# Performance work log

Hardware: AMD Instinct MI355X
Metric: run time of the kernel (lower is better)

Reference implementation:

```python
import jax, jax.numpy as jnp
import numpy as np

NUM_EXPERTS = 8
TOP_K = 2
ROUTE_SCALE = 1.0
DIM = 1024
HID = 1024
B, S = 2, 4096


def setup_inputs() -> dict:
    key = jax.random.key(0)
    ks = jax.random.split(key, 9)
    sc = 0.05
    return {
        "x": jax.random.normal(ks[0], (B, S, DIM), dtype=jnp.float32),
        "gate_w": jax.random.normal(ks[1], (NUM_EXPERTS, DIM), dtype=jnp.float32) * sc,
        "w1": jax.random.normal(ks[2], (NUM_EXPERTS, HID, DIM), dtype=jnp.float32) * sc,
        "w2": jax.random.normal(ks[3], (NUM_EXPERTS, DIM, HID), dtype=jnp.float32) * sc,
        "w3": jax.random.normal(ks[4], (NUM_EXPERTS, HID, DIM), dtype=jnp.float32) * sc,
        "sw1": jax.random.normal(ks[5], (HID, DIM), dtype=jnp.float32) * sc,
        "sw2": jax.random.normal(ks[6], (DIM, HID), dtype=jnp.float32) * sc,
        "sw3": jax.random.normal(ks[7], (HID, DIM), dtype=jnp.float32) * sc,
        "expert_bias": jnp.zeros((NUM_EXPERTS,), dtype=jnp.float32),
    }


def reference(x, gate_w, w1, w2, w3, sw1, sw2, sw3, expert_bias):
    bs, slen, dim = x.shape
    xf = x.reshape(-1, dim)                      # [T, D]

    # ---- router (sigmoid scoring, top-k over scores + bias, gather true scores) ----
    scores = jax.nn.sigmoid((xf @ gate_w.T).astype(jnp.float32))   # [T, E]
    _, sel = jax.lax.top_k(scores + expert_bias[None, :], TOP_K)    # [T, K] int32
    top_scores = jnp.take_along_axis(scores, sel, axis=1) * ROUTE_SCALE  # [T, K]

    # ---- stable sort token-slots by chosen expert (dispatch permutation) ----
    flat_sel = sel.reshape(-1)                       # [T*K]
    order = jnp.argsort(flat_sel, stable=True)       # [T*K]
    scores_sorted = top_scores.reshape(-1)[order]    # [T*K]
    tok_idx = order // TOP_K                         # source token per slot
    expert_ids = flat_sel[order]                     # sorted expert id per slot

    routed = xf[tok_idx]                             # gather [T*K, D]
    # score_before_experts=True: scale inputs by routing score
    routed = (routed.astype(jnp.float32) * scores_sorted[:, None]).astype(x.dtype)

    # ---- grouped expert GLU MLP (loop over fixed expert count, masked) ----
    out_r = jnp.zeros_like(routed)
    for e in range(NUM_EXPERTS):
        m = (expert_ids == e)[:, None]
        h = jax.nn.silu(routed @ w1[e].T) * (routed @ w3[e].T)   # [T*K, H]
        out_r = out_r + jnp.where(m, h @ w2[e].T, jnp.zeros((), routed.dtype))

    # ---- shared expert on all tokens ----
    shared = (jax.nn.silu(xf @ sw1.T) * (xf @ sw3.T)) @ sw2.T    # [T, D]

    # NOTE: original code multiplies by routing scores again after experts
    # (in addition to score_before_experts) -- replicated faithfully.
    out_r = (out_r.astype(jnp.float32) * scores_sorted[:, None]).astype(x.dtype)

    out = shared.at[tok_idx].add(out_r)              # scatter-add combine
    return out.reshape(bs, slen, dim)
```

## Files before the change

kernel.cpp:

```cpp
#include <hip/hip_runtime.h>
#include <stdint.h>

typedef unsigned short u16;
typedef unsigned int u32;

#define T_TOK 8192
#define DIMSZ 1024
#define HIDSZ 1024
#define NE 8
#define NSLOT (T_TOK * 2)
#define NPAD (NSLOT + 1024)

typedef __attribute__((ext_vector_type(8))) __bf16 bf16x8;
typedef __attribute__((ext_vector_type(16))) float f32x16;

#define MFMA32(a, b, c) __builtin_amdgcn_mfma_f32_32x32x16_bf16(a, b, c, 0, 0, 0)

__device__ __forceinline__ size_t ablk(int pos, int c) {
  return ((((size_t)(pos >> 7) * 32 + (c >> 5)) * 4 + ((c >> 3) & 3)) * 128 +
          (pos & 127)) * 8 + (c & 7);
}

__device__ __forceinline__ u16 f2bf(float f) {
  u32 u = __builtin_bit_cast(u32, f);
  u += 0x7FFFu + ((u >> 16) & 1u);
  return (u16)(u >> 16);
}
__device__ __forceinline__ float bflo(u32 v) { return __builtin_bit_cast(float, v << 16); }
__device__ __forceinline__ float bfhi(u32 v) { return __builtin_bit_cast(float, v & 0xffff0000u); }
__device__ __forceinline__ u32 pack2(float a, float b) {
  return (u32)f2bf(a) | ((u32)f2bf(b) << 16);
}
__device__ __forceinline__ float silu_f(float v) { return v / (1.f + expf(-v)); }

__device__ __forceinline__ void gload16(const void* g, void* l) {
  __builtin_amdgcn_global_load_lds(
      (const __attribute__((address_space(1))) unsigned int*)g,
      (__attribute__((address_space(3))) unsigned int*)l, 16, 0, 0);
}

#define PIPE_SYNC(N) asm volatile("s_waitcnt vmcnt(" #N ")\n\ts_barrier" ::: "memory")

__global__ __launch_bounds__(256) void convert_blocked(
    const float* __restrict__ s0, const float* __restrict__ s1,
    const float* __restrict__ s2, const float* __restrict__ ss0,
    const float* __restrict__ ss1, const float* __restrict__ ss2,
    u16* __restrict__ d0, u16* __restrict__ d1, u16* __restrict__ d2,
    u16* __restrict__ ds0, u16* __restrict__ ds1, u16* __restrict__ ds2) {
  __shared__ u16 lt[2048];
  int t = blockIdx.x;
  const float* s;
  u16* d;
  if (t < NE * 16 * 32) {
    s = (blockIdx.y == 0) ? s0 : (blockIdx.y == 1) ? s1 : s2;
    d = (blockIdx.y == 0) ? d0 : (blockIdx.y == 1) ? d1 : d2;
  } else {
    t -= NE * 16 * 32;
    s = (blockIdx.y == 0) ? ss0 : (blockIdx.y == 1) ? ss1 : ss2;
    d = (blockIdx.y == 0) ? ds0 : (blockIdx.y == 1) ? ds1 : ds2;
  }
  int rt = t >> 5, kt = t & 31;
  const float* sp = s + (size_t)rt * 64 * 1024 + kt * 32;
  int nl = threadIdx.x >> 2, k0 = (threadIdx.x & 3) * 8;
  float4 a = *(const float4*)(sp + (size_t)nl * 1024 + k0);
  float4 b = *(const float4*)(sp + (size_t)nl * 1024 + k0 + 4);
  uint4 p;
  p.x = pack2(a.x, a.y); p.y = pack2(a.z, a.w);
  p.z = pack2(b.x, b.y); p.w = pack2(b.z, b.w);
  *(uint4*)&lt[(threadIdx.x & 3) * 512 + nl * 8] = p;
  __syncthreads();
  *(uint4*)(d + (size_t)t * 2048 + threadIdx.x * 8) = *(const uint4*)&lt[threadIdx.x * 8];
}

__global__ __launch_bounds__(256) void router_kernel(
    const float* __restrict__ x, const float* __restrict__ gw,
    const float* __restrict__ bias, int* __restrict__ sel,
    float* __restrict__ selscore, u16* __restrict__ xb) {
  int t = blockIdx.x * 4 + (threadIdx.x >> 6);
  int lane = threadIdx.x & 63;
  float a[NE];
#pragma unroll
  for (int e = 0; e < NE; e++) a[e] = 0.f;
#pragma unroll
  for (int j = 0; j < 4; j++) {
    int c = j * 256 + lane * 4;
    float4 xv = *(const float4*)&x[(size_t)t * DIMSZ + c];
    uint2 p;
    p.x = pack2(xv.x, xv.y);
    p.y = pack2(xv.z, xv.w);
    *(uint2*)&xb[ablk(t, c)] = p;
#pragma unroll
    for (int e = 0; e < NE; e++) {
      float4 gv = *(const float4*)&gw[e * DIMSZ + c];
      a[e] = fmaf(xv.x, gv.x, fmaf(xv.y, gv.y, fmaf(xv.z, gv.z, fmaf(xv.w, gv.w, a[e]))));
    }
  }
#pragma unroll
  for (int off = 1; off < 64; off <<= 1)
#pragma unroll
    for (int e = 0; e < NE; e++) a[e] += __shfl_xor(a[e], off);
  if (lane == 0) {
    float s[NE], b[NE];
#pragma unroll
    for (int e = 0; e < NE; e++) {
      s[e] = 1.f / (1.f + expf(-a[e]));
      b[e] = s[e] + bias[e];
    }
    int e1 = 0; float v1 = b[0];
#pragma unroll
    for (int e = 1; e < NE; e++) if (b[e] > v1) { v1 = b[e]; e1 = e; }
    int e2 = -1; float v2 = -1e30f;
#pragma unroll
    for (int e = 0; e < NE; e++) if (e != e1 && b[e] > v2) { v2 = b[e]; e2 = e; }
    sel[t * 2] = e1; sel[t * 2 + 1] = e2;
    selscore[t * 2] = s[e1];
    selscore[t * 2 + 1] = s[e2];
  }
}

__global__ __launch_bounds__(1024) void rank_kernel(
    const int* __restrict__ sel, const float* __restrict__ selscore,
    int* __restrict__ slot2pos, float* __restrict__ slot_score,
    int* __restrict__ counts, int* __restrict__ offsets) {
  __shared__ int hist[NE * 1024];
  __shared__ int tot[NE];
  __shared__ int offs[NE];
  int tid = threadIdx.x;
  int sl[16];
  int h[NE];
#pragma unroll
  for (int e = 0; e < NE; e++) h[e] = 0;
#pragma unroll
  for (int j = 0; j < 4; j++) {
    int4 v = ((const int4*)sel)[tid * 4 + j];
    sl[j * 4 + 0] = v.x; sl[j * 4 + 1] = v.y;
    sl[j * 4 + 2] = v.z; sl[j * 4 + 3] = v.w;
  }
#pragma unroll
  for (int i = 0; i < 16; i++)
#pragma unroll
    for (int e = 0; e < NE; e++) h[e] += (sl[i] == e) ? 1 : 0;
#pragma unroll
  for (int e = 0; e < NE; e++) hist[e * 1024 + tid] = h[e];
  __syncthreads();
  int wid = tid >> 6, lane = tid & 63;
  if (wid < NE) {
    int e = wid;
    int vals[16];
    int lsum = 0;
#pragma unroll
    for (int i = 0; i < 16; i++) {
      int v = hist[e * 1024 + lane * 16 + i];
      vals[i] = lsum;
      lsum += v;
    }
    int incl = lsum;
#pragma unroll
    for (int off = 1; off < 64; off <<= 1) {
      int v = __shfl_up(incl, off);
      if (lane >= off) incl += v;
    }
    int excl = incl - lsum;
#pragma unroll
    for (int i = 0; i < 16; i++) hist[e * 1024 + lane * 16 + i] = vals[i] + excl;
    if (lane == 63) tot[e] = incl;
  }
  __syncthreads();
  if (tid == 0) {
    int acc = 0;
    for (int e = 0; e < NE; e++) {
      offs[e] = acc;
      offsets[e] = acc;
      counts[e] = tot[e];
      acc += (tot[e] + 127) & ~127;
    }
  }
  __syncthreads();
  int base[NE];
#pragma unroll
  for (int e = 0; e < NE; e++) base[e] = offs[e] + hist[e * 1024 + tid];
#pragma unroll
  for (int i = 0; i < 16; i++) {
    int slot = tid * 16 + i;
    int e = sl[i];
    int pos = 0;
#pragma unroll
    for (int k = 0; k < NE; k++) pos += (e == k) ? base[k] : 0;
#pragma unroll
    for (int k = 0; k < NE; k++) base[k] += (e == k) ? 1 : 0;
    slot2pos[slot] = pos;
    slot_score[pos] = selscore[slot];
  }
}

__global__ __launch_bounds__(256) void gather_kernel(
    const u16* __restrict__ xb, const float* __restrict__ selscore,
    const int* __restrict__ slot2pos, u16* __restrict__ routed) {
  int s = blockIdx.x * 4 + (threadIdx.x >> 6);
  int lane = threadIdx.x & 63;
  int pos = slot2pos[s];
  float sc = selscore[s];
  int t = s >> 1;
#pragma unroll
  for (int j = 0; j < 4; j++) {
    int c = j * 256 + lane * 4;
    uint2 v = *(const uint2*)&xb[ablk(t, c)];
    uint2 p;
    p.x = pack2(bflo(v.x) * sc, bfhi(v.x) * sc);
    p.y = pack2(bflo(v.y) * sc, bfhi(v.y) * sc);
    *(uint2*)&routed[ablk(pos, c)] = p;
  }
}

#define BUFE 12288

#define PIPE_STAGE(B)                                  \
  do {                                                 \
    u16* Lb = &lds[(B) * BUFE];                        \
    gload16(pAa, Lb + tid * 8);                        \
    gload16(pAa + 2048, Lb + 2048 + tid * 8);          \
    gload16(pAb, Lb + 4096 + tid * 8);                 \
    gload16(pAb + 2048, Lb + 6144 + tid * 8);          \
    gload16(pBu0, Lb + 8192 + tid * 8);                \
    gload16(pBu1, Lb + 10240 + tid * 8);               \
    pAa += 4096; pAb += 4096; pBu0 += 2048; pBu1 += 2048; \
  } while (0)

#define PIPE_COMPUTE(B)                                                  \
  do {                                                                   \
    _Pragma("unroll")                                                    \
    for (int c = 0; c < 2; c++) {                                        \
      int kc = 2 * c + l5;                                               \
      const u16* La = &lds[(B) * BUFE] + wy * 4096 + kc * 1024;          \
      const u16* Lw = &lds[(B) * BUFE] + 8192 + wn * 2048 + kc * 512;    \
      bf16x8 b0 = *(const bf16x8*)&Lw[l31 * 8];                          \
      bf16x8 b1 = *(const bf16x8*)&Lw[256 + l31 * 8];                    \
      bf16x8 a0 = *(const bf16x8*)&La[l31 * 8];                          \
      acc[0][0] = MFMA32(a0, b0, acc[0][0]);                             \
      acc[0][1] = MFMA32(a0, b1, acc[0][1]);                             \
      bf16x8 a1 = *(const bf16x8*)&La[256 + l31 * 8];                    \
      acc[1][0] = MFMA32(a1, b0, acc[1][0]);                             \
      acc[1][1] = MFMA32(a1, b1, acc[1][1]);                             \
      bf16x8 a2 = *(const bf16x8*)&La[512 + l31 * 8];                    \
      acc[2][0] = MFMA32(a2, b0, acc[2][0]);                             \
      acc[2][1] = MFMA32(a2, b1, acc[2][1]);                             \
      bf16x8 a3 = *(const bf16x8*)&La[768 + l31 * 8];                    \
      acc[3][0] = MFMA32(a3, b0, acc[3][0]);                             \
      acc[3][1] = MFMA32(a3, b1, acc[3][1]);                             \
    }                                                                    \
  } while (0)

#define PIPE_PHASE(SB, CB)                  \
  PIPE_SYNC(6);                             \
  PIPE_STAGE(SB);                           \
  __builtin_amdgcn_s_setprio(1);            \
  PIPE_COMPUTE(CB);                         \
  __builtin_amdgcn_s_setprio(0);

#define PIPE_LOOP()                         \
  PIPE_STAGE(0);                            \
  PIPE_STAGE(1);                            \
  _Pragma("unroll 1")                       \
  for (int t = 0; t < 30; t += 3) {         \
    PIPE_PHASE(2, 0);                       \
    PIPE_PHASE(0, 1);                       \
    PIPE_PHASE(1, 2);                       \
  }                                         \
  PIPE_SYNC(6);                             \
  __builtin_amdgcn_s_setprio(1);            \
  PIPE_COMPUTE(0);                          \
  __builtin_amdgcn_s_setprio(0);            \
  PIPE_SYNC(0);                             \
  __builtin_amdgcn_s_setprio(1);            \
  PIPE_COMPUTE(1);                          \
  __builtin_amdgcn_s_setprio(0);

__global__ __launch_bounds__(256, 2) void dual_glu_gemm(
    const u16* __restrict__ A, const u16* __restrict__ W1,
    const u16* __restrict__ W3, u16* __restrict__ Hout,
    const u16* __restrict__ As, const u16* __restrict__ SW1,
    const u16* __restrict__ SW3, u16* __restrict__ Hs,
    const int* __restrict__ seg_off, const int* __restrict__ seg_cnt) {
  int flat = blockIdx.x + 16 * blockIdx.y + 512 * blockIdx.z;
  int xcd = flat & 7;
  int r = flat >> 3;
  int bx = r & 15;
  int s = r >> 4;
  int z, by;
  if (s < 4) { z = NE; by = xcd * 4 + s; }
  else       { z = xcd; by = s - 4; }

  const u16 *Ap, *w1p, *w3p;
  u16* Hp;
  int soff, scnt;
  if (z < NE) {
    soff = seg_off[z]; scnt = seg_cnt[z];
    Ap = A;
    w1p = W1 + (size_t)z * HIDSZ * DIMSZ;
    w3p = W3 + (size_t)z * HIDSZ * DIMSZ;
    Hp = Hout;
  } else {
    soff = 0; scnt = T_TOK;
    Ap = As; w1p = SW1; w3p = SW3;
    Hp = Hs;
  }
  int mbase = by * 256;
  if (mbase >= scnt) return;
  int hx = bx;

  __shared__ u16 lds[3 * BUFE];

  int tid = threadIdx.x;
  int lane = tid & 63;
  int wid = tid >> 6;
  int wy = wid >> 1, wn = wid & 1;
  int l5 = lane >> 5, l31 = lane & 31;

  const u16* pAa = Ap + (size_t)((soff + mbase) >> 7) * 32 * 4096 + tid * 8;
  const u16* pAb = pAa + 32 * 4096;
  const u16* pBu0 = w1p + (size_t)hx * 32 * 2048 + tid * 8;
  const u16* pBu1 = w3p + (size_t)hx * 32 * 2048 + tid * 8;

  f32x16 acc[4][2];
#pragma unroll
  for (int i = 0; i < 4; i++) { acc[i][0] = (f32x16)0.f; acc[i][1] = (f32x16)0.f; }

  PIPE_LOOP();

  __syncthreads();
  float* ex = (float*)lds;
  if (wn == 0) {
#pragma unroll
    for (int i = 0; i < 4; i++)
#pragma unroll
      for (int j = 0; j < 2; j++)
#pragma unroll
        for (int r2 = 0; r2 < 16; r2++) {
          int rowl = i * 32 + (r2 & 3) + 8 * (r2 >> 2) + 4 * l5;
          ex[(wy * 128 + rowl) * 64 + j * 32 + l31] = acc[i][j][r2];
        }
  }
  __syncthreads();
  if (wn == 1) {
#pragma unroll
    for (int i = 0; i < 4; i++)
#pragma unroll
      for (int j = 0; j < 2; j++)
#pragma unroll
        for (int r2 = 0; r2 < 16; r2++) {
          int rowl = i * 32 + (r2 & 3) + 8 * (r2 >> 2) + 4 * l5;
          int grow = mbase + wy * 128 + rowl;
          if (grow < scnt) {
            float h1 = ex[(wy * 128 + rowl) * 64 + j * 32 + l31];
            Hp[ablk(soff + grow, hx * 64 + j * 32 + l31)] =
                f2bf(silu_f(h1) * acc[i][j][r2]);
          }
        }
  }
}

__global__ __launch_bounds__(256, 2) void gemm2_kernel(
    const u16* __restrict__ A, const u16* __restrict__ W, u16* __restrict__ OutB,
    const u16* __restrict__ As, const u16* __restrict__ SW, float* __restrict__ OutF,
    const float* __restrict__ scale, const int* __restrict__ seg_off,
    const int* __restrict__ seg_cnt) {
  int flat = blockIdx.x + 8 * blockIdx.y + 256 * blockIdx.z;
  int xcd = flat & 7;
  int r = flat >> 3;
  int bx = r & 7;
  int s = r >> 3;
  int z, by;
  if (s < 4) { z = NE; by = xcd * 4 + s; }
  else       { z = xcd; by = s - 4; }

  const u16 *Ap, *wp;
  int soff, scnt;
  if (z < NE) {
    soff = seg_off[z]; scnt = seg_cnt[z];
    Ap = A; wp = W + (size_t)z * DIMSZ * HIDSZ;
  } else {
    soff = 0; scnt = T_TOK;
    Ap = As; wp = SW;
  }
  int mbase = by * 256;
  if (mbase >= scnt) return;
  int nbase = bx * 128;

  __shared__ u16 lds[3 * BUFE];

  int tid = threadIdx.x;
  int lane = tid & 63;
  int wid = tid >> 6;
  int wy = wid >> 1, wn = wid & 1;
  int l5 = lane >> 5, l31 = lane & 31;

  const u16* pAa = Ap + (size_t)((soff + mbase) >> 7) * 32 * 4096 + tid * 8;
  const u16* pAb = pAa + 32 * 4096;
  const u16* pBu0 = wp + (size_t)(nbase >> 6) * 32 * 2048 + tid * 8;
  const u16* pBu1 = pBu0 + 32 * 2048;

  f32x16 acc[4][2];
#pragma unroll
  for (int i = 0; i < 4; i++) { acc[i][0] = (f32x16)0.f; acc[i][1] = (f32x16)0.f; }

  PIPE_LOOP();

#pragma unroll
  for (int i = 0; i < 4; i++)
#pragma unroll
    for (int j = 0; j < 2; j++) {
      int colg = nbase + wn * 64 + j * 32 + l31;
#pragma unroll
      for (int r2 = 0; r2 < 16; r2++) {
        int rowl = (r2 & 3) + 8 * (r2 >> 2) + 4 * l5;
        int grow = mbase + wy * 128 + i * 32 + rowl;
        if (grow < scnt) {
          size_t idx = (size_t)(soff + grow) * DIMSZ + colg;
          if (z < NE) {
            OutB[idx] = f2bf(acc[i][j][r2] * scale[soff + grow]);
          } else {
            OutF[idx] = acc[i][j][r2];
          }
        }
      }
    }
}

__global__ __launch_bounds__(256) void combine_kernel(
    float* __restrict__ out, const u16* __restrict__ Orb,
    const int* __restrict__ slot2pos) {
  int t = blockIdx.x;
  int d = threadIdx.x * 4;
  int p0 = slot2pos[t * 2];
  int p1 = slot2pos[t * 2 + 1];
  float4 o = *(float4*)&out[(size_t)t * DIMSZ + d];
  uint2 a = *(const uint2*)&Orb[(size_t)p0 * DIMSZ + d];
  uint2 b = *(const uint2*)&Orb[(size_t)p1 * DIMSZ + d];
  o.x += bflo(a.x) + bflo(b.x);
  o.y += bfhi(a.x) + bfhi(b.x);
  o.z += bflo(a.y) + bflo(b.y);
  o.w += bfhi(a.y) + bfhi(b.y);
  *(float4*)&out[(size_t)t * DIMSZ + d] = o;
}

extern "C" void kernel_launch(void* const* d_in, const int* in_sizes, int n_in,
                              void* d_out, int out_size, void* d_ws, size_t ws_size,
                              hipStream_t stream) {
  const float* x = (const float*)d_in[0];
  const float* gw = (const float*)d_in[1];
  const float* w1 = (const float*)d_in[2];
  const float* w2 = (const float*)d_in[3];
  const float* w3 = (const float*)d_in[4];
  const float* sw1 = (const float*)d_in[5];
  const float* sw2 = (const float*)d_in[6];
  const float* sw3 = (const float*)d_in[7];
  const float* bias = (const float*)d_in[8];
  float* out = (float*)d_out;

  uint8_t* ws = (uint8_t*)d_ws;
  size_t off = 0;
  auto alloc = [&](size_t b) { size_t o = off; off += (b + 255) & ~(size_t)255; return o; };

  size_t ctrl = alloc(256);
  int* counts = (int*)(ws + ctrl);
  int* offsets = counts + 16;
  int* sel = (int*)(ws + alloc((size_t)NSLOT * 4));
  float* selscore = (float*)(ws + alloc((size_t)NSLOT * 4));
  float* slot_score = (float*)(ws + alloc((size_t)NPAD * 4));
  int* slot2pos = (int*)(ws + alloc((size_t)NSLOT * 4));
  u16* xb = (u16*)(ws + alloc((size_t)T_TOK * DIMSZ * 2));
  u16* routed = (u16*)(ws + alloc((size_t)NPAD * DIMSZ * 2));
  u16* Hbuf = (u16*)(ws + alloc((size_t)NPAD * HIDSZ * 2));
  u16* Orb = (u16*)(ws + alloc((size_t)NPAD * DIMSZ * 2));
  u16* Hs = (u16*)(ws + alloc((size_t)T_TOK * HIDSZ * 2));
  u16* w1b = (u16*)(ws + alloc((size_t)NE * HIDSZ * DIMSZ * 2));
  u16* w2b = (u16*)(ws + alloc((size_t)NE * DIMSZ * HIDSZ * 2));
  u16* w3b = (u16*)(ws + alloc((size_t)NE * HIDSZ * DIMSZ * 2));
  u16* sw1b = (u16*)(ws + alloc((size_t)HIDSZ * DIMSZ * 2));
  u16* sw2b = (u16*)(ws + alloc((size_t)DIMSZ * HIDSZ * 2));
  u16* sw3b = (u16*)(ws + alloc((size_t)HIDSZ * DIMSZ * 2));

  convert_blocked<<<dim3((NE + 1) * 16 * 32, 3), 256, 0, stream>>>(
      w1, w2, w3, sw1, sw2, sw3, w1b, w2b, w3b, sw1b, sw2b, sw3b);

  router_kernel<<<T_TOK / 4, 256, 0, stream>>>(x, gw, bias, sel, selscore, xb);
  rank_kernel<<<1, 1024, 0, stream>>>(sel, selscore, slot2pos, slot_score,
                                      counts, offsets);
  gather_kernel<<<NSLOT / 4, 256, 0, stream>>>(xb, selscore, slot2pos, routed);

  dual_glu_gemm<<<dim3(16, 32, NE + 1), 256, 0, stream>>>(
      routed, w1b, w3b, Hbuf, xb, sw1b, sw3b, Hs, offsets, counts);
  gemm2_kernel<<<dim3(8, 32, NE + 1), 256, 0, stream>>>(
      Hbuf, w2b, Orb, Hs, sw2b, out, slot_score, offsets, counts);

  combine_kernel<<<T_TOK, 256, 0, stream>>>(out, Orb, slot2pos);
}
```

Measured before the change: 595.6 us.

## Split GEMM tiles across 8 waves with 512-thread blocks, halving per-wave accumulators

Both grouped GEMM kernels now launch 512 threads (8 waves) per 256x128 tile instead of 256 threads (4 waves). Each wave computes a 64x64 sub-tile with 4 MFMA accumulators instead of 8, and each thread issues 3 global-to-LDS loads per stage instead of 6. The pipeline wait count drops to match. This frees registers and adds waves to hide latency, at the cost of one block per CU instead of two and more A-fragment LDS reads per MFMA.

```diff
diff --git a/kernel.cpp b/kernel.cpp
--- a/kernel.cpp
+++ b/kernel.cpp
@@ -218,12 +218,9 @@
   do {                                                 \
     u16* Lb = &lds[(B) * BUFE];                        \
     gload16(pAa, Lb + tid * 8);                        \
-    gload16(pAa + 2048, Lb + 2048 + tid * 8);          \
     gload16(pAb, Lb + 4096 + tid * 8);                 \
-    gload16(pAb + 2048, Lb + 6144 + tid * 8);          \
-    gload16(pBu0, Lb + 8192 + tid * 8);                \
-    gload16(pBu1, Lb + 10240 + tid * 8);               \
-    pAa += 4096; pAb += 4096; pBu0 += 2048; pBu1 += 2048; \
+    gload16(pBm, Lb + 8192 + (tid >> 8) * 2048 + (tid & 255) * 8); \
+    pAa += 4096; pAb += 4096; pBm += 2048;             \
   } while (0)
 
 #define PIPE_COMPUTE(B)                                                  \
@@ -231,7 +228,8 @@
     _Pragma("unroll")                                                    \
     for (int c = 0; c < 2; c++) {                                        \
       int kc = 2 * c + l5;                                               \
-      const u16* La = &lds[(B) * BUFE] + wy * 4096 + kc * 1024;          \
+      const u16* La = &lds[(B) * BUFE] + (wy >> 1) * 4096 + kc * 1024 +  \
+                      (wy & 1) * 512;                                    \
       const u16* Lw = &lds[(B) * BUFE] + 8192 + wn * 2048 + kc * 512;    \
       bf16x8 b0 = *(const bf16x8*)&Lw[l31 * 8];                          \
       bf16x8 b1 = *(const bf16x8*)&Lw[256 + l31 * 8];                    \
@@ -241,17 +239,11 @@
       bf16x8 a1 = *(const bf16x8*)&La[256 + l31 * 8];                    \
       acc[1][0] = MFMA32(a1, b0, acc[1][0]);                             \
       acc[1][1] = MFMA32(a1, b1, acc[1][1]);                             \
-      bf16x8 a2 = *(const bf16x8*)&La[512 + l31 * 8];                    \
-      acc[2][0] = MFMA32(a2, b0, acc[2][0]);                             \
-      acc[2][1] = MFMA32(a2, b1, acc[2][1]);                             \
-      bf16x8 a3 = *(const bf16x8*)&La[768 + l31 * 8];                    \
-      acc[3][0] = MFMA32(a3, b0, acc[3][0]);                             \
-      acc[3][1] = MFMA32(a3, b1, acc[3][1]);                             \
     }                                                                    \
   } while (0)
 
 #define PIPE_PHASE(SB, CB)                  \
-  PIPE_SYNC(6);                             \
+  PIPE_SYNC(3);                             \
   PIPE_STAGE(SB);                           \
   __builtin_amdgcn_s_setprio(1);            \
   PIPE_COMPUTE(CB);                         \
@@ -266,7 +258,7 @@
     PIPE_PHASE(0, 1);                       \
     PIPE_PHASE(1, 2);                       \
   }                                         \
-  PIPE_SYNC(6);                             \
+  PIPE_SYNC(3);                             \
   __builtin_amdgcn_s_setprio(1);            \
   PIPE_COMPUTE(0);                          \
   __builtin_amdgcn_s_setprio(0);            \
@@ -275,7 +267,7 @@
   PIPE_COMPUTE(1);                          \
   __builtin_amdgcn_s_setprio(0);
 
-__global__ __launch_bounds__(256, 2) void dual_glu_gemm(
+__global__ __launch_bounds__(512, 1) void dual_glu_gemm(
     const u16* __restrict__ A, const u16* __restrict__ W1,
     const u16* __restrict__ W3, u16* __restrict__ Hout,
     const u16* __restrict__ As, const u16* __restrict__ SW1,
@@ -318,12 +310,12 @@
 
   const u16* pAa = Ap + (size_t)((soff + mbase) >> 7) * 32 * 4096 + tid * 8;
   const u16* pAb = pAa + 32 * 4096;
-  const u16* pBu0 = w1p + (size_t)hx * 32 * 2048 + tid * 8;
-  const u16* pBu1 = w3p + (size_t)hx * 32 * 2048 + tid * 8;
-
-  f32x16 acc[4][2];
-#pragma unroll
-  for (int i = 0; i < 4; i++) { acc[i][0] = (f32x16)0.f; acc[i][1] = (f32x16)0.f; }
+  const u16* pBm = ((tid >> 8) == 0 ? w1p : w3p) +
+                   (size_t)hx * 32 * 2048 + (tid & 255) * 8;
+
+  f32x16 acc[2][2];
+  acc[0][0] = (f32x16)0.f; acc[0][1] = (f32x16)0.f;
+  acc[1][0] = (f32x16)0.f; acc[1][1] = (f32x16)0.f;
 
   PIPE_LOOP();
 
@@ -331,27 +323,27 @@
   float* ex = (float*)lds;
   if (wn == 0) {
 #pragma unroll
-    for (int i = 0; i < 4; i++)
+    for (int i = 0; i < 2; i++)
 #pragma unroll
       for (int j = 0; j < 2; j++)
 #pragma unroll
         for (int r2 = 0; r2 < 16; r2++) {
-          int rowl = i * 32 + (r2 & 3) + 8 * (r2 >> 2) + 4 * l5;
-          ex[(wy * 128 + rowl) * 64 + j * 32 + l31] = acc[i][j][r2];
+          int rowl = wy * 64 + i * 32 + (r2 & 3) + 8 * (r2 >> 2) + 4 * l5;
+          ex[rowl * 64 + j * 32 + l31] = acc[i][j][r2];
         }
   }
   __syncthreads();
   if (wn == 1) {
 #pragma unroll
-    for (int i = 0; i < 4; i++)
+    for (int i = 0; i < 2; i++)
 #pragma unroll
       for (int j = 0; j < 2; j++)
 #pragma unroll
         for (int r2 = 0; r2 < 16; r2++) {
-          int rowl = i * 32 + (r2 & 3) + 8 * (r2 >> 2) + 4 * l5;
-          int grow = mbase + wy * 128 + rowl;
+          int rowl = wy * 64 + i * 32 + (r2 & 3) + 8 * (r2 >> 2) + 4 * l5;
+          int grow = mbase + rowl;
           if (grow < scnt) {
-            float h1 = ex[(wy * 128 + rowl) * 64 + j * 32 + l31];
+            float h1 = ex[rowl * 64 + j * 32 + l31];
             Hp[ablk(soff + grow, hx * 64 + j * 32 + l31)] =
                 f2bf(silu_f(h1) * acc[i][j][r2]);
           }
@@ -359,7 +351,7 @@
   }
 }
 
-__global__ __launch_bounds__(256, 2) void gemm2_kernel(
+__global__ __launch_bounds__(512, 1) void gemm2_kernel(
     const u16* __restrict__ A, const u16* __restrict__ W, u16* __restrict__ OutB,
     const u16* __restrict__ As, const u16* __restrict__ SW, float* __restrict__ OutF,
     const float* __restrict__ scale, const int* __restrict__ seg_off,
@@ -396,24 +388,24 @@
 
   const u16* pAa = Ap + (size_t)((soff + mbase) >> 7) * 32 * 4096 + tid * 8;
   const u16* pAb = pAa + 32 * 4096;
-  const u16* pBu0 = wp + (size_t)(nbase >> 6) * 32 * 2048 + tid * 8;
-  const u16* pBu1 = pBu0 + 32 * 2048;
-
-  f32x16 acc[4][2];
-#pragma unroll
-  for (int i = 0; i < 4; i++) { acc[i][0] = (f32x16)0.f; acc[i][1] = (f32x16)0.f; }
+  const u16* pBm = wp + (size_t)((nbase >> 6) + (tid >> 8)) * 32 * 2048 +
+                   (tid & 255) * 8;
+
+  f32x16 acc[2][2];
+  acc[0][0] = (f32x16)0.f; acc[0][1] = (f32x16)0.f;
+  acc[1][0] = (f32x16)0.f; acc[1][1] = (f32x16)0.f;
 
   PIPE_LOOP();
 
 #pragma unroll
-  for (int i = 0; i < 4; i++)
+  for (int i = 0; i < 2; i++)
 #pragma unroll
     for (int j = 0; j < 2; j++) {
       int colg = nbase + wn * 64 + j * 32 + l31;
 #pragma unroll
       for (int r2 = 0; r2 < 16; r2++) {
         int rowl = (r2 & 3) + 8 * (r2 >> 2) + 4 * l5;
-        int grow = mbase + wy * 128 + i * 32 + rowl;
+        int grow = mbase + wy * 64 + i * 32 + rowl;
         if (grow < scnt) {
           size_t idx = (size_t)(soff + grow) * DIMSZ + colg;
           if (z < NE) {
@@ -488,9 +480,9 @@
                                       counts, offsets);
   gather_kernel<<<NSLOT / 4, 256, 0, stream>>>(xb, selscore, slot2pos, routed);
 
-  dual_glu_gemm<<<dim3(16, 32, NE + 1), 256, 0, stream>>>(
+  dual_glu_gemm<<<dim3(16, 32, NE + 1), 512, 0, stream>>>(
       routed, w1b, w3b, Hbuf, xb, sw1b, sw3b, Hs, offsets, counts);
-  gemm2_kernel<<<dim3(8, 32, NE + 1), 256, 0, stream>>>(
+  gemm2_kernel<<<dim3(8, 32, NE + 1), 512, 0, stream>>>(
       Hbuf, w2b, Orb, Hs, sw2b, out, slot_score, offsets, counts);
 
   combine_kernel<<<T_TOK, 256, 0, stream>>>(out, Orb, slot2pos);
```

After: 486.5 us. 18.3% less time.

## Widen GEMM tiles to 256x256 with 512-thread blocks for more A reuse

Applied to the files above, without the earlier changes.

Both grouped GEMM kernels move from 256-thread blocks with 256x128 output tiles to 512-thread blocks with 256x256 tiles (8 waves in a 2x4 layout). Each staged A tile now feeds twice as many output columns, and the B loads are remapped so each thread issues fewer loads per stage. The intent is to roughly halve A-operand global and LDS traffic per unit of compute. The GLU epilogue is rewritten into two passes that exchange results through LDS. LDS per block grows to three 32KB buffers, and with 512 threads and launch_bounds(512,2) register pressure and occupancy may suffer.

```diff
diff --git a/kernel.cpp b/kernel.cpp
--- a/kernel.cpp
+++ b/kernel.cpp
@@ -212,18 +212,16 @@
   }
 }
 
-#define BUFE 12288
-
-#define PIPE_STAGE(B)                                  \
-  do {                                                 \
-    u16* Lb = &lds[(B) * BUFE];                        \
-    gload16(pAa, Lb + tid * 8);                        \
-    gload16(pAa + 2048, Lb + 2048 + tid * 8);          \
-    gload16(pAb, Lb + 4096 + tid * 8);                 \
-    gload16(pAb + 2048, Lb + 6144 + tid * 8);          \
-    gload16(pBu0, Lb + 8192 + tid * 8);                \
-    gload16(pBu1, Lb + 10240 + tid * 8);               \
-    pAa += 4096; pAb += 4096; pBu0 += 2048; pBu1 += 2048; \
+#define BUFE 16384
+
+#define PIPE_STAGE(B)                                          \
+  do {                                                         \
+    u16* Lb = &lds[(B) * BUFE];                                \
+    gload16(pAa, Lb + tid * 8);                                \
+    gload16(pAb, Lb + 4096 + tid * 8);                         \
+    gload16(pBm, Lb + 8192 + bu * 2048 + bi * 8);              \
+    gload16(pBm + 1024, Lb + 9216 + bu * 2048 + bi * 8);       \
+    pAa += 4096; pAb += 4096; pBm += 2048;                     \
   } while (0)
 
 #define PIPE_COMPUTE(B)                                                  \
@@ -251,7 +249,7 @@
   } while (0)
 
 #define PIPE_PHASE(SB, CB)                  \
-  PIPE_SYNC(6);                             \
+  PIPE_SYNC(4);                             \
   PIPE_STAGE(SB);                           \
   __builtin_amdgcn_s_setprio(1);            \
   PIPE_COMPUTE(CB);                         \
@@ -266,7 +264,7 @@
     PIPE_PHASE(0, 1);                       \
     PIPE_PHASE(1, 2);                       \
   }                                         \
-  PIPE_SYNC(6);                             \
+  PIPE_SYNC(4);                             \
   __builtin_amdgcn_s_setprio(1);            \
   PIPE_COMPUTE(0);                          \
   __builtin_amdgcn_s_setprio(0);            \
@@ -275,17 +273,17 @@
   PIPE_COMPUTE(1);                          \
   __builtin_amdgcn_s_setprio(0);
 
-__global__ __launch_bounds__(256, 2) void dual_glu_gemm(
+__global__ __launch_bounds__(512, 2) void dual_glu_gemm(
     const u16* __restrict__ A, const u16* __restrict__ W1,
     const u16* __restrict__ W3, u16* __restrict__ Hout,
     const u16* __restrict__ As, const u16* __restrict__ SW1,
     const u16* __restrict__ SW3, u16* __restrict__ Hs,
     const int* __restrict__ seg_off, const int* __restrict__ seg_cnt) {
-  int flat = blockIdx.x + 16 * blockIdx.y + 512 * blockIdx.z;
+  int flat = blockIdx.x + 8 * blockIdx.y + 256 * blockIdx.z;
   int xcd = flat & 7;
   int r = flat >> 3;
-  int bx = r & 15;
-  int s = r >> 4;
+  int bx = r & 7;
+  int s = r >> 3;
   int z, by;
   if (s < 4) { z = NE; by = xcd * 4 + s; }
   else       { z = xcd; by = s - 4; }
@@ -313,13 +311,14 @@
   int tid = threadIdx.x;
   int lane = tid & 63;
   int wid = tid >> 6;
-  int wy = wid >> 1, wn = wid & 1;
+  int wy = wid >> 2, wn = wid & 3;
   int l5 = lane >> 5, l31 = lane & 31;
+  int bu = tid >> 7, bi = tid & 127;
 
   const u16* pAa = Ap + (size_t)((soff + mbase) >> 7) * 32 * 4096 + tid * 8;
   const u16* pAb = pAa + 32 * 4096;
-  const u16* pBu0 = w1p + (size_t)hx * 32 * 2048 + tid * 8;
-  const u16* pBu1 = w3p + (size_t)hx * 32 * 2048 + tid * 8;
+  const u16* pBm = ((bu < 2) ? w1p : w3p) +
+                   (size_t)(hx * 2 + (bu & 1)) * 32 * 2048 + bi * 8;
 
   f32x16 acc[4][2];
 #pragma unroll
@@ -327,48 +326,50 @@
 
   PIPE_LOOP();
 
-  __syncthreads();
   float* ex = (float*)lds;
-  if (wn == 0) {
-#pragma unroll
-    for (int i = 0; i < 4; i++)
-#pragma unroll
-      for (int j = 0; j < 2; j++)
-#pragma unroll
-        for (int r2 = 0; r2 < 16; r2++) {
-          int rowl = i * 32 + (r2 & 3) + 8 * (r2 >> 2) + 4 * l5;
-          ex[(wy * 128 + rowl) * 64 + j * 32 + l31] = acc[i][j][r2];
-        }
-  }
-  __syncthreads();
-  if (wn == 1) {
-#pragma unroll
-    for (int i = 0; i < 4; i++)
-#pragma unroll
-      for (int j = 0; j < 2; j++)
-#pragma unroll
-        for (int r2 = 0; r2 < 16; r2++) {
-          int rowl = i * 32 + (r2 & 3) + 8 * (r2 >> 2) + 4 * l5;
-          int grow = mbase + wy * 128 + rowl;
-          if (grow < scnt) {
-            float h1 = ex[(wy * 128 + rowl) * 64 + j * 32 + l31];
-            Hp[ablk(soff + grow, hx * 64 + j * 32 + l31)] =
-                f2bf(silu_f(h1) * acc[i][j][r2]);
+  for (int rr = 0; rr < 2; rr++) {
+    __syncthreads();
+    if (wy == rr && wn < 2) {
+#pragma unroll
+      for (int i = 0; i < 4; i++)
+#pragma unroll
+        for (int j = 0; j < 2; j++)
+#pragma unroll
+          for (int r2 = 0; r2 < 16; r2++) {
+            int rowl = i * 32 + (r2 & 3) + 8 * (r2 >> 2) + 4 * l5;
+            ex[rowl * 128 + wn * 64 + j * 32 + l31] = acc[i][j][r2];
           }
-        }
-  }
-}
-
-__global__ __launch_bounds__(256, 2) void gemm2_kernel(
+    }
+    __syncthreads();
+    if (wy == rr && wn >= 2) {
+#pragma unroll
+      for (int i = 0; i < 4; i++)
+#pragma unroll
+        for (int j = 0; j < 2; j++)
+#pragma unroll
+          for (int r2 = 0; r2 < 16; r2++) {
+            int rowl = i * 32 + (r2 & 3) + 8 * (r2 >> 2) + 4 * l5;
+            int grow = mbase + rr * 128 + rowl;
+            if (grow < scnt) {
+              float h1 = ex[rowl * 128 + (wn - 2) * 64 + j * 32 + l31];
+              Hp[ablk(soff + grow, hx * 128 + (wn - 2) * 64 + j * 32 + l31)] =
+                  f2bf(silu_f(h1) * acc[i][j][r2]);
+            }
+          }
+    }
+  }
+}
+
+__global__ __launch_bounds__(512, 2) void gemm2_kernel(
     const u16* __restrict__ A, const u16* __restrict__ W, u16* __restrict__ OutB,
     const u16* __restrict__ As, const u16* __restrict__ SW, float* __restrict__ OutF,
     const float* __restrict__ scale, const int* __restrict__ seg_off,
     const int* __restrict__ seg_cnt) {
-  int flat = blockIdx.x + 8 * blockIdx.y + 256 * blockIdx.z;
+  int flat = blockIdx.x + 4 * blockIdx.y + 128 * blockIdx.z;
   int xcd = flat & 7;
   int r = flat >> 3;
-  int bx = r & 7;
-  int s = r >> 3;
+  int bx = r & 3;
+  int s = r >> 2;
   int z, by;
   if (s < 4) { z = NE; by = xcd * 4 + s; }
   else       { z = xcd; by = s - 4; }
@@ -384,20 +385,20 @@
   }
   int mbase = by * 256;
   if (mbase >= scnt) return;
-  int nbase = bx * 128;
+  int nbase = bx * 256;
 
   __shared__ u16 lds[3 * BUFE];
 
   int tid = threadIdx.x;
   int lane = tid & 63;
   int wid = tid >> 6;
-  int wy = wid >> 1, wn = wid & 1;
+  int wy = wid >> 2, wn = wid & 3;
   int l5 = lane >> 5, l31 = lane & 31;
+  int bu = tid >> 7, bi = tid & 127;
 
   const u16* pAa = Ap + (size_t)((soff + mbase) >> 7) * 32 * 4096 + tid * 8;
   const u16* pAb = pAa + 32 * 4096;
-  const u16* pBu0 = wp + (size_t)(nbase >> 6) * 32 * 2048 + tid * 8;
-  const u16* pBu1 = pBu0 + 32 * 2048;
+  const u16* pBm = wp + (size_t)((nbase >> 6) + bu) * 32 * 2048 + bi * 8;
 
   f32x16 acc[4][2];
 #pragma unroll
@@ -488,9 +489,9 @@
                                       counts, offsets);
   gather_kernel<<<NSLOT / 4, 256, 0, stream>>>(xb, selscore, slot2pos, routed);
 
-  dual_glu_gemm<<<dim3(16, 32, NE + 1), 256, 0, stream>>>(
+  dual_glu_gemm<<<dim3(8, 32, NE + 1), 512, 0, stream>>>(
       routed, w1b, w3b, Hbuf, xb, sw1b, sw3b, Hs, offsets, counts);
-  gemm2_kernel<<<dim3(8, 32, NE + 1), 256, 0, stream>>>(
+  gemm2_kernel<<<dim3(4, 32, NE + 1), 512, 0, stream>>>(
       Hbuf, w2b, Orb, Hs, sw2b, out, slot_score, offsets, counts);
 
   combine_kernel<<<T_TOK, 256, 0, stream>>>(out, Orb, slot2pos);
```

Result: slower. 792.1 us (+33.0%).
